# Performance work log

Hardware: AMD Instinct MI355X
Metric: run time of the kernel (lower is better)

Reference implementation:

```python
import jax, jax.numpy as jnp
import numpy as np

N_NODES = 10000
N_EDGES = 320000
D_FEAT = 128          # per-node feature dim -> in_dim = 2*D_FEAT = 256
OUT_DIM = 128
SCALES = 3


def setup_inputs() -> dict:
    key = jax.random.key(0)
    ks = jax.random.split(key, 7)
    node_features = jax.random.normal(ks[0], (N_NODES, D_FEAT), dtype=jnp.float32)
    temporal_info = jax.random.normal(ks[1], (N_NODES,), dtype=jnp.float32)
    in_dim_p1 = 2 * D_FEAT + 1  # 257: concat(src, dest) + temporal gap
    W1 = jax.random.normal(ks[2], (SCALES, in_dim_p1, OUT_DIM), dtype=jnp.float32) * 0.05
    b1 = jax.random.normal(ks[3], (SCALES, OUT_DIM), dtype=jnp.float32) * 0.05
    W2 = jax.random.normal(ks[4], (SCALES, OUT_DIM, OUT_DIM), dtype=jnp.float32) * 0.05
    b2 = jax.random.normal(ks[5], (SCALES, OUT_DIM), dtype=jnp.float32) * 0.05
    edge_index = jax.random.randint(ks[6], (2, N_EDGES), 0, N_NODES, dtype=jnp.int64)
    return {
        "node_features": node_features,
        "temporal_info": temporal_info,
        "W1": W1, "b1": b1, "W2": W2, "b2": b2,
        "edge_index": edge_index,
    }


def reference(node_features, temporal_info, W1, b1, W2, b2, edge_index):
    src, dest = edge_index[0], edge_index[1]
    # gather node pairs + temporal gap -> [E, 2*D+1]
    gap = (temporal_info[src] - temporal_info[dest])[:, None]
    edge_features = jnp.concatenate(
        [node_features[src], node_features[dest], gap], axis=-1)
    # all scales' 2-layer MLPs in one batched einsum; s = scale axis
    h = jax.nn.relu(jnp.einsum('ef,sfo->seo', edge_features, W1) + b1[:, None, :])
    tokens = jnp.einsum('seo,sop->sep', h, W2) + b2[:, None, :]  # [S, E, OUT]
    return tokens.mean(axis=0)  # mean over scales -> [E, OUT]
```

## Files before the change

### kernel.cpp

```cpp
#include <hip/hip_runtime.h>
#include <stdint.h>

#define NN 10000
#define NE 320000
#define DF 128
#define OD 128
#define NS 3

typedef __attribute__((ext_vector_type(8))) short bf16x8;
typedef __attribute__((ext_vector_type(16))) float f32x16;

static __device__ __forceinline__ uint32_t f2bf(float f) {
  uint32_t u = __float_as_uint(f);
  return (u + 0x7FFFu + ((u >> 16) & 1u)) >> 16;
}
static __device__ __forceinline__ float bflo(uint32_t u) { return __uint_as_float(u << 16); }
static __device__ __forceinline__ float bfhi(uint32_t u) { return __uint_as_float(u & 0xFFFF0000u); }

static __device__ __forceinline__ uint32_t relu2(uint32_t a, uint32_t d) {
  float f0 = fmaxf(bflo(a) + bflo(d), 0.0f);
  float f1 = fmaxf(bfhi(a) + bfhi(d), 0.0f);
  return f2bf(f0) | (f2bf(f1) << 16);
}

static __device__ __forceinline__ void lds_barrier() {
  asm volatile("s_waitcnt lgkmcnt(0)" ::: "memory");
  __builtin_amdgcn_s_barrier();
}

__global__ __launch_bounds__(256) void prep_w2(
    const float* __restrict__ W2, const float* __restrict__ b2,
    unsigned short* __restrict__ w2f, float* __restrict__ bmean)
{
  int o = blockIdx.x * 256 + threadIdx.x;
  if (o < NS * 8 * 256 * 8) {
    int j = o & 7;
    int t = (o >> 3) & 255;
    int q = (o >> 11) & 7;
    int s = o >> 14;
    int w = t >> 6, lane = t & 63;
    int n = w * 32 + (lane & 31);
    int k = q * 16 + (lane >> 5) * 8 + j;
    w2f[o] = (unsigned short)f2bf(W2[((size_t)s * OD + k) * OD + n]);
  }
  if (o < OD) bmean[o] = (b2[o] + b2[OD + o] + b2[2 * OD + o]) * (1.0f / 3.0f);
}

__global__ __launch_bounds__(256) void node_proj(
    const float* __restrict__ nf, const float* __restrict__ temporal,
    const float* __restrict__ W1, const float* __restrict__ b1,
    unsigned short* __restrict__ Qsrc, unsigned short* __restrict__ Qdst)
{
  __shared__ unsigned short Asm[8 * 64 * 8];
  __shared__ unsigned short Bsm[4 * 8 * 64 * 8];
  __shared__ float tsh[32];

  const int t = threadIdx.x;
  const int c = blockIdx.y;
  const int s = c >> 1, proj = c & 1;

  {
    int o = t & 127, qh = t >> 7;
    const float* wbase = W1 + (size_t)(s * 257 + proj * 128) * OD + o;
    int nt = o >> 5, lnlo = o & 31;
    #pragma unroll
    for (int r = 0; r < 8; r++) {
      int kh = qh * 8 + r;
      float v[8];
      #pragma unroll
      for (int j = 0; j < 8; j++) v[j] = wbase[(size_t)(kh * 8 + j) * OD];
      uint32_t pk[4];
      #pragma unroll
      for (int i = 0; i < 4; i++) pk[i] = f2bf(v[2 * i]) | (f2bf(v[2 * i + 1]) << 16);
      int q = kh >> 1, half = kh & 1;
      uint32_t* d = (uint32_t*)(Bsm + ((nt * 8 + q) * 64 + half * 32 + lnlo) * 8);
      d[0] = pk[0]; d[1] = pk[1]; d[2] = pk[2]; d[3] = pk[3];
    }
  }

  const int lane = t & 63, w = t >> 6;
  const int o = w * 32 + (lane & 31);
  const float w1gv = W1[(size_t)(s * 257 + 256) * OD + o];
  const float b1v = b1[s * OD + o];
  unsigned short* Qt = (proj == 0) ? Qsrc : Qdst;
  const int m = t >> 3, j16 = t & 7;

  for (int it = 0; it < 8; it++) {
    const int m0 = (blockIdx.x * 8 + it) * 32;
    if (m0 >= NN) break;

    if (t < 32) tsh[t] = (m0 + t < NN) ? temporal[m0 + t] : 0.0f;

    {
      int node = m0 + m;
      float v[16];
      if (node < NN) {
        const float4* p = (const float4*)(nf + (size_t)node * DF + j16 * 16);
        #pragma unroll
        for (int i = 0; i < 4; i++) {
          float4 x = p[i];
          v[4 * i] = x.x; v[4 * i + 1] = x.y; v[4 * i + 2] = x.z; v[4 * i + 3] = x.w;
        }
      } else {
        #pragma unroll
        for (int i = 0; i < 16; i++) v[i] = 0.0f;
      }
      uint32_t pk[8];
      #pragma unroll
      for (int i = 0; i < 8; i++) pk[i] = f2bf(v[2 * i]) | (f2bf(v[2 * i + 1]) << 16);
      uint32_t* d0 = (uint32_t*)(Asm + (j16 * 64 + (m ^ j16)) * 8);
      uint32_t* d1 = (uint32_t*)(Asm + (j16 * 64 + ((32 + m) ^ j16)) * 8);
      d0[0] = pk[0]; d0[1] = pk[1]; d0[2] = pk[2]; d0[3] = pk[3];
      d1[0] = pk[4]; d1[1] = pk[5]; d1[2] = pk[6]; d1[3] = pk[7];
    }
    __syncthreads();

    f32x16 C;
    #pragma unroll
    for (int i = 0; i < 16; i++) C[i] = 0.0f;
    #pragma unroll
    for (int q = 0; q < 8; q++) {
      bf16x8 a = *(const bf16x8*)(Asm + (q * 64 + (lane ^ q)) * 8);
      bf16x8 b = *(const bf16x8*)(Bsm + ((w * 8 + q) * 64 + lane) * 8);
      C = __builtin_amdgcn_mfma_f32_32x32x16_bf16(a, b, C, 0, 0, 0);
    }

    #pragma unroll
    for (int r = 0; r < 16; r++) {
      int row = (r & 3) + 8 * (r >> 2) + 4 * (lane >> 5);
      int node = m0 + row;
      if (node < NN) {
        float val = C[r];
        if (proj == 0) val += b1v + tsh[row] * w1gv;
        else           val -= tsh[row] * w1gv;
        Qt[(size_t)node * (NS * OD) + s * OD + o] = (unsigned short)f2bf(val);
      }
    }
    __syncthreads();
  }
}

__global__ __launch_bounds__(256, 4) void edge_mlp(
    const unsigned short* __restrict__ Qsrc, const unsigned short* __restrict__ Qdst,
    const unsigned short* __restrict__ W2F, const float* __restrict__ bmean,
    const int* __restrict__ ei, float* __restrict__ out)
{
  __shared__ unsigned short hsm[NS * 8 * 64 * 8];

  const int t = threadIdx.x;
  const int lane = t & 63, w = t >> 6;
  const int nlo = lane & 31, khi = lane >> 5;
  const float bmv = bmean[w * 32 + nlo];
  const int m = t >> 3, j16 = t & 7;

  const unsigned short* pw0 = W2F + (size_t)t * 8;

  int snn = ei[blockIdx.x * 128 + m];
  int dnn = ei[NE + blockIdx.x * 128 + m];

  #pragma unroll 1
  for (int tt = 0; tt < 4; tt++) {
    const int e0 = blockIdx.x * 128 + tt * 32;
    const int sn = snn, dn = dnn;

    if (tt < 3) {
      snn = ei[e0 + 32 + m];
      dnn = ei[NE + e0 + 32 + m];
    }

    uint4 G[12];
    {
      const unsigned short* ps = Qsrc + (size_t)sn * (NS * OD) + j16 * 16;
      const unsigned short* pd = Qdst + (size_t)dn * (NS * OD) + j16 * 16;
      #pragma unroll
      for (int s = 0; s < NS; s++) {
        G[4 * s + 0] = *(const uint4*)(ps + s * OD);
        G[4 * s + 1] = *(const uint4*)(ps + s * OD + 8);
        G[4 * s + 2] = *(const uint4*)(pd + s * OD);
        G[4 * s + 3] = *(const uint4*)(pd + s * OD + 8);
      }
    }

    #pragma unroll
    for (int s = 0; s < NS; s++) {
      uint4 a0 = G[4 * s + 0], a1 = G[4 * s + 1];
      uint4 d0 = G[4 * s + 2], d1 = G[4 * s + 3];
      uint4 w0, w1;
      w0.x = relu2(a0.x, d0.x); w0.y = relu2(a0.y, d0.y);
      w0.z = relu2(a0.z, d0.z); w0.w = relu2(a0.w, d0.w);
      w1.x = relu2(a1.x, d1.x); w1.y = relu2(a1.y, d1.y);
      w1.z = relu2(a1.z, d1.z); w1.w = relu2(a1.w, d1.w);
      *(uint4*)(hsm + ((s * 8 + j16) * 64 + (m ^ j16)) * 8) = w0;
      *(uint4*)(hsm + ((s * 8 + j16) * 64 + ((32 + m) ^ j16)) * 8) = w1;
    }

    const unsigned short* pw = pw0;
    asm volatile("" : "+v"(pw));
    bf16x8 fA[8], fB[8], fC[8];
    #pragma unroll
    for (int q = 0; q < 8; q++) fA[q] = *(const bf16x8*)(pw + (0 * 8 + q) * 2048);
    #pragma unroll
    for (int q = 0; q < 8; q++) fB[q] = *(const bf16x8*)(pw + (1 * 8 + q) * 2048);
    #pragma unroll
    for (int q = 0; q < 8; q++) fC[q] = *(const bf16x8*)(pw + (2 * 8 + q) * 2048);

    lds_barrier();

    f32x16 C;
    #pragma unroll
    for (int i = 0; i < 16; i++) C[i] = 0.0f;
    __builtin_amdgcn_s_setprio(1);
    #pragma unroll
    for (int q = 0; q < 8; q++) {
      bf16x8 a = *(const bf16x8*)(hsm + ((0 * 8 + q) * 64 + (lane ^ q)) * 8);
      C = __builtin_amdgcn_mfma_f32_32x32x16_bf16(a, fA[q], C, 0, 0, 0);
    }
    #pragma unroll
    for (int q = 0; q < 8; q++) {
      bf16x8 a = *(const bf16x8*)(hsm + ((1 * 8 + q) * 64 + (lane ^ q)) * 8);
      C = __builtin_amdgcn_mfma_f32_32x32x16_bf16(a, fB[q], C, 0, 0, 0);
    }
    #pragma unroll
    for (int q = 0; q < 8; q++) {
      bf16x8 a = *(const bf16x8*)(hsm + ((2 * 8 + q) * 64 + (lane ^ q)) * 8);
      C = __builtin_amdgcn_mfma_f32_32x32x16_bf16(a, fC[q], C, 0, 0, 0);
    }
    __builtin_amdgcn_s_setprio(0);

    #pragma unroll
    for (int r = 0; r < 16; r++) {
      int row = (r & 3) + 8 * (r >> 2) + 4 * khi;
      __builtin_nontemporal_store(C[r] * (1.0f / 3.0f) + bmv,
          &out[(size_t)(e0 + row) * OD + w * 32 + nlo]);
    }
    lds_barrier();
  }
}

extern "C" void kernel_launch(void* const* d_in, const int* in_sizes, int n_in,
                              void* d_out, int out_size, void* d_ws, size_t ws_size,
                              hipStream_t stream) {
  const float* nf       = (const float*)d_in[0];
  const float* temporal = (const float*)d_in[1];
  const float* W1       = (const float*)d_in[2];
  const float* b1       = (const float*)d_in[3];
  const float* W2       = (const float*)d_in[4];
  const float* b2       = (const float*)d_in[5];
  const int*   ei       = (const int*)d_in[6];
  float* out = (float*)d_out;

  char* ws = (char*)d_ws;
  unsigned short* Qsrc = (unsigned short*)ws;
  unsigned short* Qdst = (unsigned short*)(ws + 7680000);
  unsigned short* W2F  = (unsigned short*)(ws + 15360000);
  float*          bmv  = (float*)(ws + 15360000 + 98304);

  prep_w2 <<<dim3(192),    dim3(256), 0, stream>>>(W2, b2, W2F, bmv);
  node_proj<<<dim3(40, 6), dim3(256), 0, stream>>>(nf, temporal, W1, b1, Qsrc, Qdst);
  edge_mlp <<<dim3(2500),  dim3(256), 0, stream>>>(Qsrc, Qdst, W2F, bmv, ei, out);
}
```

Measured before the change: 295.8 us.

## Bucket-sort edges by node block for gather locality with XCD-aware block remap

Adds a counting-sort pass (histogram, scan, scatter) that groups edges into 2D buckets keyed by the 512-node blocks of their source and destination, so the edge MLP gathers projected node rows from a smaller working set. Blocks are remapped so that each XCD processes a contiguous range of sorted edges and L2 locality improves. Outputs are written back to the original edge positions through a permutation array, which makes the stores scattered by row. The cost is three to four extra small kernels plus atomics, and the sort order is nondeterministic within a bucket, which does not change results.

```diff
diff --git a/kernel.cpp b/kernel.cpp
--- a/kernel.cpp
+++ b/kernel.cpp
@@ -7,6 +7,8 @@
 #define OD 128
 #define NS 3
 
+#define NBK 400
+
 typedef __attribute__((ext_vector_type(8))) short bf16x8;
 typedef __attribute__((ext_vector_type(16))) float f32x16;
 
@@ -21,6 +23,11 @@
   float f0 = fmaxf(bflo(a) + bflo(d), 0.0f);
   float f1 = fmaxf(bfhi(a) + bfhi(d), 0.0f);
   return f2bf(f0) | (f2bf(f1) << 16);
+}
+
+static __device__ __forceinline__ int bkey(int s, int d) {
+  int sb = s >> 9, db = d >> 9;
+  return ((sb >> 2) * 5 + (db >> 2)) * 16 + (sb & 3) * 4 + (db & 3);
 }
 
 static __device__ __forceinline__ void lds_barrier() {
@@ -140,10 +147,61 @@
   }
 }
 
+__global__ __launch_bounds__(256) void zero_aux(int* __restrict__ gh) {
+  int t = blockIdx.x * 256 + threadIdx.x;
+  if (t < NBK) gh[t] = 0;
+}
+
+__global__ __launch_bounds__(256) void edge_hist(
+    const int* __restrict__ ei, int* __restrict__ gh)
+{
+  __shared__ int h[NBK];
+  for (int i = threadIdx.x; i < NBK; i += 256) h[i] = 0;
+  __syncthreads();
+  int e = blockIdx.x * 256 + threadIdx.x;
+  if (e < NE) {
+    int s = ei[e], d = ei[NE + e];
+    atomicAdd(&h[bkey(s, d)], 1);
+  }
+  __syncthreads();
+  for (int i = threadIdx.x; i < NBK; i += 256)
+    if (h[i]) atomicAdd(&gh[i], h[i]);
+}
+
+__global__ __launch_bounds__(512) void bucket_scan(
+    const int* __restrict__ gh, int* __restrict__ cursor)
+{
+  __shared__ int sc[512];
+  int t = threadIdx.x;
+  int own = (t < NBK) ? gh[t] : 0;
+  sc[t] = own;
+  __syncthreads();
+  for (int off = 1; off < 512; off <<= 1) {
+    int add = (t >= off) ? sc[t - off] : 0;
+    int v = sc[t];
+    __syncthreads();
+    sc[t] = v + add;
+    __syncthreads();
+  }
+  if (t < NBK) cursor[t] = sc[t] - own;
+}
+
+__global__ __launch_bounds__(256) void edge_scatter(
+    const int* __restrict__ ei, int* __restrict__ cursor,
+    int* __restrict__ es, int* __restrict__ ed, int* __restrict__ eo)
+{
+  int e = blockIdx.x * 256 + threadIdx.x;
+  if (e >= NE) return;
+  int s = ei[e], d = ei[NE + e];
+  int pos = atomicAdd(&cursor[bkey(s, d)], 1);
+  es[pos] = s; ed[pos] = d; eo[pos] = e;
+}
+
 __global__ __launch_bounds__(256, 4) void edge_mlp(
     const unsigned short* __restrict__ Qsrc, const unsigned short* __restrict__ Qdst,
     const unsigned short* __restrict__ W2F, const float* __restrict__ bmean,
-    const int* __restrict__ ei, float* __restrict__ out)
+    const int* __restrict__ es, const int* __restrict__ ed,
+    const int* __restrict__ eo, float* __restrict__ out)
 {
   __shared__ unsigned short hsm[NS * 8 * 64 * 8];
 
@@ -153,20 +211,32 @@
   const float bmv = bmean[w * 32 + nlo];
   const int m = t >> 3, j16 = t & 7;
 
+  int bid;
+  {
+    int orig = blockIdx.x;
+    int xcd = orig & 7, rank = orig >> 3;
+    bid = (xcd < 4) ? xcd * 313 + rank : 4 * 313 + (xcd - 4) * 312 + rank;
+  }
+
   const unsigned short* pw0 = W2F + (size_t)t * 8;
 
-  int snn = ei[blockIdx.x * 128 + m];
-  int dnn = ei[NE + blockIdx.x * 128 + m];
+  int snn = es[bid * 128 + m];
+  int dnn = ed[bid * 128 + m];
 
   #pragma unroll 1
   for (int tt = 0; tt < 4; tt++) {
-    const int e0 = blockIdx.x * 128 + tt * 32;
+    const int e0 = bid * 128 + tt * 32;
     const int sn = snn, dn = dnn;
 
     if (tt < 3) {
-      snn = ei[e0 + 32 + m];
-      dnn = ei[NE + e0 + 32 + m];
-    }
+      snn = es[e0 + 32 + m];
+      dnn = ed[e0 + 32 + m];
+    }
+
+    int eor[16];
+    #pragma unroll
+    for (int r = 0; r < 16; r++)
+      eor[r] = eo[e0 + ((r & 3) + 8 * (r >> 2) + 4 * khi)];
 
     uint4 G[12];
     {
@@ -229,9 +299,8 @@
 
     #pragma unroll
     for (int r = 0; r < 16; r++) {
-      int row = (r & 3) + 8 * (r >> 2) + 4 * khi;
       __builtin_nontemporal_store(C[r] * (1.0f / 3.0f) + bmv,
-          &out[(size_t)(e0 + row) * OD + w * 32 + nlo]);
+          &out[(size_t)eor[r] * OD + w * 32 + nlo]);
     }
     lds_barrier();
   }
@@ -253,9 +322,18 @@
   unsigned short* Qsrc = (unsigned short*)ws;
   unsigned short* Qdst = (unsigned short*)(ws + 7680000);
   unsigned short* W2F  = (unsigned short*)(ws + 15360000);
-  float*          bmv  = (float*)(ws + 15360000 + 98304);
-
-  prep_w2 <<<dim3(192),    dim3(256), 0, stream>>>(W2, b2, W2F, bmv);
-  node_proj<<<dim3(40, 6), dim3(256), 0, stream>>>(nf, temporal, W1, b1, Qsrc, Qdst);
-  edge_mlp <<<dim3(2500),  dim3(256), 0, stream>>>(Qsrc, Qdst, W2F, bmv, ei, out);
-}
+  float*          bmv  = (float*)(ws + 15458304);
+  int*            gh   = (int*)(ws + 15458816);
+  int*            cur  = (int*)(ws + 15460416);
+  int*            es   = (int*)(ws + 15462016);
+  int*            ed   = (int*)(ws + 16742016);
+  int*            eo   = (int*)(ws + 18022016);
+
+  prep_w2     <<<dim3(192),    dim3(256), 0, stream>>>(W2, b2, W2F, bmv);
+  zero_aux    <<<dim3(2),      dim3(256), 0, stream>>>(gh);
+  node_proj   <<<dim3(40, 6),  dim3(256), 0, stream>>>(nf, temporal, W1, b1, Qsrc, Qdst);
+  edge_hist   <<<dim3(1250),   dim3(256), 0, stream>>>(ei, gh);
+  bucket_scan <<<dim3(1),      dim3(512), 0, stream>>>(gh, cur);
+  edge_scatter<<<dim3(1250),   dim3(256), 0, stream>>>(ei, cur, es, ed, eo);
+  edge_mlp    <<<dim3(2500),   dim3(256), 0, stream>>>(Qsrc, Qdst, W2F, bmv, es, ed, eo, out);
+}
```

Result: slower. 445.5 us (+50.6%).

## Restructure edge MLP per-wave over 32 edges with double-buffered scale gathers

Applied to the files above, without the earlier changes.

Each wavefront now owns 32 edges and computes all four 32-column output blocks, instead of four waves sharing 32 edges per iteration. Per-scale hidden tiles are double-buffered in wave-private LDS, so the gather for the next scale overlaps the MFMAs of the current one and block-wide barriers disappear. The trade-off is higher register pressure (four accumulators, launch bounds lowered to 2) and more LDS per block. W2 fragments are also reloaded from global memory inside the inner loop, and the output stores are no longer non-temporal.

```diff
diff --git a/kernel.cpp b/kernel.cpp
--- a/kernel.cpp
+++ b/kernel.cpp
@@ -21,11 +21,6 @@
   float f0 = fmaxf(bflo(a) + bflo(d), 0.0f);
   float f1 = fmaxf(bfhi(a) + bfhi(d), 0.0f);
   return f2bf(f0) | (f2bf(f1) << 16);
-}
-
-static __device__ __forceinline__ void lds_barrier() {
-  asm volatile("s_waitcnt lgkmcnt(0)" ::: "memory");
-  __builtin_amdgcn_s_barrier();
 }
 
 __global__ __launch_bounds__(256) void prep_w2(
@@ -140,100 +135,94 @@
   }
 }
 
-__global__ __launch_bounds__(256, 4) void edge_mlp(
+__global__ __launch_bounds__(256, 2) void edge_mlp(
     const unsigned short* __restrict__ Qsrc, const unsigned short* __restrict__ Qdst,
     const unsigned short* __restrict__ W2F, const float* __restrict__ bmean,
     const int* __restrict__ ei, float* __restrict__ out)
 {
-  __shared__ unsigned short hsm[NS * 8 * 64 * 8];
+  __shared__ unsigned short hsm[4][2][8 * 64 * 8];
 
   const int t = threadIdx.x;
   const int lane = t & 63, w = t >> 6;
-  const int nlo = lane & 31, khi = lane >> 5;
-  const float bmv = bmean[w * 32 + nlo];
-  const int m = t >> 3, j16 = t & 7;
-
-  const unsigned short* pw0 = W2F + (size_t)t * 8;
-
-  int snn = ei[blockIdx.x * 128 + m];
-  int dnn = ei[NE + blockIdx.x * 128 + m];
-
-  #pragma unroll 1
-  for (int tt = 0; tt < 4; tt++) {
-    const int e0 = blockIdx.x * 128 + tt * 32;
-    const int sn = snn, dn = dnn;
-
-    if (tt < 3) {
-      snn = ei[e0 + 32 + m];
-      dnn = ei[NE + e0 + 32 + m];
-    }
-
-    uint4 G[12];
-    {
-      const unsigned short* ps = Qsrc + (size_t)sn * (NS * OD) + j16 * 16;
-      const unsigned short* pd = Qdst + (size_t)dn * (NS * OD) + j16 * 16;
-      #pragma unroll
-      for (int s = 0; s < NS; s++) {
-        G[4 * s + 0] = *(const uint4*)(ps + s * OD);
-        G[4 * s + 1] = *(const uint4*)(ps + s * OD + 8);
-        G[4 * s + 2] = *(const uint4*)(pd + s * OD);
-        G[4 * s + 3] = *(const uint4*)(pd + s * OD + 8);
+  const int e0 = (blockIdx.x * 4 + w) * 32;
+  const int r31 = lane & 31;
+  const int esub = lane >> 4;
+  const int p = lane & 15;
+  const int j = p >> 1, kh = p & 1;
+
+  const int sn = ei[e0 + r31];
+  const int dn = ei[NE + e0 + r31];
+
+  float bm[4];
+  #pragma unroll
+  for (int nb = 0; nb < 4; nb++) bm[nb] = bmean[nb * 32 + r31];
+
+  unsigned short* buf0 = hsm[w][0];
+  unsigned short* buf1 = hsm[w][1];
+
+  uint4 ga[8], gd[8];
+
+#define GLOAD(S) do {                                                         \
+    _Pragma("unroll") for (int b = 0; b < 8; b++) {                           \
+      int se = __shfl(sn, 4 * b + esub);                                      \
+      int de = __shfl(dn, 4 * b + esub);                                      \
+      ga[b] = *(const uint4*)(Qsrc + (size_t)se * (NS * OD) + (S) * OD + p * 8); \
+      gd[b] = *(const uint4*)(Qdst + (size_t)de * (NS * OD) + (S) * OD + p * 8); \
+    } } while (0)
+
+#define GWRITE(BUF) do {                                                      \
+    _Pragma("unroll") for (int b = 0; b < 8; b++) {                           \
+      uint4 h;                                                                \
+      h.x = relu2(ga[b].x, gd[b].x); h.y = relu2(ga[b].y, gd[b].y);           \
+      h.z = relu2(ga[b].z, gd[b].z); h.w = relu2(ga[b].w, gd[b].w);           \
+      int e = 4 * b + esub;                                                   \
+      *(uint4*)((BUF) + ((size_t)j * 64 + ((kh * 32 + e) ^ j)) * 8) = h;      \
+    } } while (0)
+
+  f32x16 C[4];
+  #pragma unroll
+  for (int nb = 0; nb < 4; nb++)
+    #pragma unroll
+    for (int i = 0; i < 16; i++) C[nb][i] = 0.0f;
+
+  GLOAD(0);
+  GWRITE(buf0);
+
+  #pragma unroll
+  for (int s = 0; s < NS; s++) {
+    unsigned short* cb   = (s & 1) ? buf1 : buf0;
+    unsigned short* nbuf = (s & 1) ? buf0 : buf1;
+
+    if (s == 0) GLOAD(1);
+    else if (s == 1) GLOAD(2);
+
+    bf16x8 af[8];
+    #pragma unroll
+    for (int q = 0; q < 8; q++)
+      af[q] = *(const bf16x8*)(cb + (q * 64 + (lane ^ q)) * 8);
+
+    #pragma unroll
+    for (int nb = 0; nb < 4; nb++) {
+      #pragma unroll
+      for (int q = 0; q < 8; q++) {
+        bf16x8 bf = *(const bf16x8*)(W2F +
+            (size_t)((((s * 8 + q) * 4 + nb) * 64 + lane)) * 8);
+        C[nb] = __builtin_amdgcn_mfma_f32_32x32x16_bf16(af[q], bf, C[nb], 0, 0, 0);
       }
     }
 
-    #pragma unroll
-    for (int s = 0; s < NS; s++) {
-      uint4 a0 = G[4 * s + 0], a1 = G[4 * s + 1];
-      uint4 d0 = G[4 * s + 2], d1 = G[4 * s + 3];
-      uint4 w0, w1;
-      w0.x = relu2(a0.x, d0.x); w0.y = relu2(a0.y, d0.y);
-      w0.z = relu2(a0.z, d0.z); w0.w = relu2(a0.w, d0.w);
-      w1.x = relu2(a1.x, d1.x); w1.y = relu2(a1.y, d1.y);
-      w1.z = relu2(a1.z, d1.z); w1.w = relu2(a1.w, d1.w);
-      *(uint4*)(hsm + ((s * 8 + j16) * 64 + (m ^ j16)) * 8) = w0;
-      *(uint4*)(hsm + ((s * 8 + j16) * 64 + ((32 + m) ^ j16)) * 8) = w1;
-    }
-
-    const unsigned short* pw = pw0;
-    asm volatile("" : "+v"(pw));
-    bf16x8 fA[8], fB[8], fC[8];
-    #pragma unroll
-    for (int q = 0; q < 8; q++) fA[q] = *(const bf16x8*)(pw + (0 * 8 + q) * 2048);
-    #pragma unroll
-    for (int q = 0; q < 8; q++) fB[q] = *(const bf16x8*)(pw + (1 * 8 + q) * 2048);
-    #pragma unroll
-    for (int q = 0; q < 8; q++) fC[q] = *(const bf16x8*)(pw + (2 * 8 + q) * 2048);
-
-    lds_barrier();
-
-    f32x16 C;
-    #pragma unroll
-    for (int i = 0; i < 16; i++) C[i] = 0.0f;
-    __builtin_amdgcn_s_setprio(1);
-    #pragma unroll
-    for (int q = 0; q < 8; q++) {
-      bf16x8 a = *(const bf16x8*)(hsm + ((0 * 8 + q) * 64 + (lane ^ q)) * 8);
-      C = __builtin_amdgcn_mfma_f32_32x32x16_bf16(a, fA[q], C, 0, 0, 0);
-    }
-    #pragma unroll
-    for (int q = 0; q < 8; q++) {
-      bf16x8 a = *(const bf16x8*)(hsm + ((1 * 8 + q) * 64 + (lane ^ q)) * 8);
-      C = __builtin_amdgcn_mfma_f32_32x32x16_bf16(a, fB[q], C, 0, 0, 0);
-    }
-    #pragma unroll
-    for (int q = 0; q < 8; q++) {
-      bf16x8 a = *(const bf16x8*)(hsm + ((2 * 8 + q) * 64 + (lane ^ q)) * 8);
-      C = __builtin_amdgcn_mfma_f32_32x32x16_bf16(a, fC[q], C, 0, 0, 0);
-    }
-    __builtin_amdgcn_s_setprio(0);
-
+    if (s < 2) GWRITE(nbuf);
+  }
+#undef GLOAD
+#undef GWRITE
+
+  #pragma unroll
+  for (int nb = 0; nb < 4; nb++) {
     #pragma unroll
     for (int r = 0; r < 16; r++) {
-      int row = (r & 3) + 8 * (r >> 2) + 4 * khi;
-      __builtin_nontemporal_store(C[r] * (1.0f / 3.0f) + bmv,
-          &out[(size_t)(e0 + row) * OD + w * 32 + nlo]);
-    }
-    lds_barrier();
+      int row = (r & 3) + 8 * (r >> 2) + 4 * (lane >> 5);
+      out[(size_t)(e0 + row) * OD + nb * 32 + r31] = C[nb][r] * (1.0f / 3.0f) + bm[nb];
+    }
   }
 }
 
@@ -255,7 +244,7 @@
   unsigned short* W2F  = (unsigned short*)(ws + 15360000);
   float*          bmv  = (float*)(ws + 15360000 + 98304);
 
-  prep_w2 <<<dim3(192),    dim3(256), 0, stream>>>(W2, b2, W2F, bmv);
-  node_proj<<<dim3(40, 6), dim3(256), 0, stream>>>(nf, temporal, W1, b1, Qsrc, Qdst);
-  edge_mlp <<<dim3(2500),  dim3(256), 0, stream>>>(Qsrc, Qdst, W2F, bmv, ei, out);
-}
+  prep_w2  <<<dim3(192),    dim3(256), 0, stream>>>(W2, b2, W2F, bmv);
+  node_proj<<<dim3(40, 6),  dim3(256), 0, stream>>>(nf, temporal, W1, b1, Qsrc, Qdst);
+  edge_mlp <<<dim3(2500),   dim3(256), 0, stream>>>(Qsrc, Qdst, W2F, bmv, ei, out);
+}
```

Result: no change. 299.9 us (+1.4%).
